# Optimization experiments

Hardware: AMD Instinct MI355X
Metric: run time of the kernel (lower is better)

The kernel has to match this reference:

```python
import jax, jax.numpy as jnp
import numpy as np

B, N, E, L, S = 8, 64, 256, 128, 2  # graphs, nodes, edges, latent dim, MPN steps


def setup_inputs() -> dict:
    key = jax.random.key(0)
    ks = jax.random.split(key, 16)

    def lin(k, fi, fo):
        return (jax.random.normal(k, (fi, fo), jnp.float32) / np.sqrt(fi).astype(np.float32))

    return {
        "x": jax.random.normal(ks[0], (B, N, L), jnp.float32),
        "edge_attr": jax.random.normal(ks[1], (B, E, L), jnp.float32),
        "u": jax.random.normal(ks[2], (B, L), jnp.float32),
        "spdist": jax.random.uniform(ks[3], (B, N, N), jnp.float32),
        "edge_index": jax.random.randint(ks[4], (B, 2, E), 0, N),
        # encoders
        "W_node_enc": lin(ks[5], 2 * L + 1, L), "b_node_enc": jnp.zeros(L, jnp.float32),
        "W_edge_enc": lin(ks[6], L, L), "b_edge_enc": jnp.zeros(L, jnp.float32),
        "W_glob_enc": lin(ks[7], L, L), "b_glob_enc": jnp.zeros(L, jnp.float32),
        # per-step edge / node update MLPs (stacked over S steps)
        "W_edge_upd": jnp.stack([lin(ks[8 + s], 4 * L, L) for s in range(S)]),
        "b_edge_upd": jnp.zeros((S, L), jnp.float32),
        "W_node_upd": jnp.stack([lin(ks[10 + s], 3 * L, L) for s in range(S)]),
        "b_node_upd": jnp.zeros((S, L), jnp.float32),
        # final edge scorer (per_dest_embedding_to_score)
        "W_score": lin(ks[12], L, 1), "b_score": jnp.zeros(1, jnp.float32),
    }


def reference(x, edge_attr, u, spdist, edge_index,
              W_node_enc, b_node_enc, W_edge_enc, b_edge_enc,
              W_glob_enc, b_glob_enc, W_edge_upd, b_edge_upd,
              W_node_upd, b_node_upd, W_score, b_score):
    act = jax.nn.leaky_relu  # torch LeakyReLU default slope 0.01
    n_steps = W_edge_upd.shape[0]

    def per_graph(xg, eg, ug, sdg, eig):
        Ng, Lg = xg.shape
        Eg = eg.shape[0]
        src, dst = eig[0], eig[1]
        # Augmented node features: graph copy d, node i -> [x_i, x_d, spdist[d, i]]
        # (matches x.repeat(N,1) / x.repeat_interleave(N,0) + chunk(N))
        x_tile = jnp.broadcast_to(xg[None, :, :], (Ng, Ng, Lg))
        x_dest = jnp.broadcast_to(xg[:, None, :], (Ng, Ng, Lg))
        xa = jnp.concatenate([x_tile, x_dest, sdg[..., None]], axis=-1)  # [Nd, N, 2L+1]
        h = act(xa @ W_node_enc + b_node_enc)                            # [Nd, N, L]
        ee = act(eg @ W_edge_enc + b_edge_enc)                           # [E, L]
        ee = jnp.broadcast_to(ee[None], (Ng, Eg, Lg))                    # [Nd, E, L]
        gg = act(ug @ W_glob_enc + b_glob_enc)                           # [L]
        for s in range(n_steps):
            gb_e = jnp.broadcast_to(gg, (Ng, Eg, Lg))
            ein = jnp.concatenate([ee, h[:, src], h[:, dst], gb_e], axis=-1)  # [Nd, E, 4L]
            ee = ee + act(ein @ W_edge_upd[s] + b_edge_upd[s])
            agg = jax.vmap(lambda ef: jax.ops.segment_sum(ef, dst, num_segments=Ng))(ee)  # [Nd, N, L]
            gb_n = jnp.broadcast_to(gg, (Ng, Ng, Lg))
            nin = jnp.concatenate([h, agg, gb_n], axis=-1)                    # [Nd, N, 3L]
            h = h + act(nin @ W_node_upd[s] + b_node_upd[s])
        scores = (ee @ W_score + b_score)[..., 0]  # [Nd, E]
        # reshape(N, -1).t().flatten() per graph -> [E * N]
        return scores.T.reshape(-1)

    out = jax.vmap(per_graph)(x, edge_attr, u, spdist, edge_index)  # [B, E*N]
    return out.reshape(-1)
```

## Files before the change

### kernel.cpp

```cpp
#include <hip/hip_runtime.h>
#include <hip/hip_bf16.h>


typedef __attribute__((ext_vector_type(8))) __bf16 bf16x8;
typedef __attribute__((ext_vector_type(4))) __bf16 bf16x4;
typedef __attribute__((ext_vector_type(4))) float  floatx4;

#define MFMA16(a, b, c) __builtin_amdgcn_mfma_f32_16x16x32_bf16((a), (b), (c), 0, 0, 0)

__device__ __forceinline__ float leaky(float x) { return x > 0.f ? x : 0.01f * x; }

#define WS_WT     0
#define WS_XAP    327680
#define WS_XDP    589824
#define WS_EE0    851968
#define WS_CE     1376256
#define WS_CN     1384448
#define WS_CSROFF 1392640
#define WS_CSREID 1394944

#define LDE 140

__global__ __launch_bounds__(256) void mpn_prep(
    const float* __restrict__ x,
    const float* __restrict__ ea,
    const float* __restrict__ u,
    const int*   __restrict__ eidx,
    const float* __restrict__ Wne,
    const float* __restrict__ bne,
    const float* __restrict__ Wee,
    const float* __restrict__ bee,
    const float* __restrict__ Wge,
    const float* __restrict__ bge,
    const float* __restrict__ Weu,
    const float* __restrict__ beu,
    const float* __restrict__ Wnu,
    const float* __restrict__ bnu,
    char* __restrict__ ws)
{
  __shared__ __align__(16) __bf16 smem[384 * LDE];

  const int b = blockIdx.x, tid = threadIdx.x;
  __bf16* wt  = (__bf16*)(ws + WS_WT);
  float*  xap = (float*)(ws + WS_XAP);
  float*  xdp = (float*)(ws + WS_XDP);
  __bf16* ee0 = (__bf16*)(ws + WS_EE0);
  float*  cev = (float*)(ws + WS_CE);
  float*  cnv = (float*)(ws + WS_CN);
  int* csroff = (int*)(ws + WS_CSROFF);
  int* csreid = (int*)(ws + WS_CSREID);

  if (b < 20) {
    const int m = b >> 1, half = b & 1;
    const int s = m / 5, t = m % 5;
    const float* src = (t < 3) ? (Weu + (size_t)(s*512 + t*128)*128)
                               : (Wnu + (size_t)(s*384 + (t-3)*128)*128);
    for (int it = 0; it < 4; ++it) {
      int p = it*256 + tid;
      int mq = half*4 + (p >> 8);
      int c  = (p >> 6) & 3;
      int l  = p & 63;
      int fr = mq*16 + (l & 15);
      int kb = c*32 + (l >> 4)*8;
      __bf16* dst = &wt[m*16384 + ((mq*4 + c)*64 + l)*8];
      #pragma unroll
      for (int j = 0; j < 8; ++j)
        dst[j] = (__bf16)src[(kb + j)*128 + fr];
    }
  } else if (b < 28) {
    const int g = b - 20;
    __shared__ float gg_sh[128];
    __shared__ int dst_sh[256];
    __shared__ int cnt_sh[64];
    __shared__ int off_sh[65];
    if (tid < 128) {
      float acc = bge[tid];
      for (int k = 0; k < 128; ++k)
        acc += u[g*128 + k] * Wge[k*128 + tid];
      gg_sh[tid] = leaky(acc);
    }
    dst_sh[tid] = eidx[g*512 + 256 + tid];
    __syncthreads();
    {
      const int s = tid >> 7, f = tid & 127;
      float ac = beu[s*128 + f];
      float an = bnu[s*128 + f];
      #pragma unroll 8
      for (int k = 0; k < 128; ++k) {
        float gk = gg_sh[k];
        ac += gk * Weu[(s*512 + 384 + k)*128 + f];
        an += gk * Wnu[(s*384 + 256 + k)*128 + f];
      }
      cev[(g*2 + s)*128 + f] = ac;
      cnv[(g*2 + s)*128 + f] = an;
    }
    if (tid < 64) {
      int c = 0;
      for (int e = 0; e < 256; ++e) c += (dst_sh[e] == tid) ? 1 : 0;
      cnt_sh[tid] = c;
    }
    __syncthreads();
    if (tid == 0) {
      int o = 0;
      for (int n = 0; n < 64; ++n) { off_sh[n] = o; o += cnt_sh[n]; }
      off_sh[64] = o;
    }
    __syncthreads();
    if (tid < 65) csroff[g*72 + tid] = off_sh[tid];
    if (tid < 64) {
      int o = off_sh[tid];
      for (int e = 0; e < 256; ++e)
        if (dst_sh[e] == tid) csreid[g*256 + (o++)] = e;
    }
  } else if (b < 36) {
    const int g = b - 28;
    __bf16* s_a = smem;
    __bf16* s_w = smem + 256*LDE;
    #pragma unroll
    for (int it = 0; it < 32; ++it) {
      int c = it*256 + tid;
      int row = c >> 5, f4 = (c & 31)*4;
      floatx4 v = *(const floatx4*)&ea[(size_t)(g*256 + row)*128 + f4];
      bf16x4 o;
      #pragma unroll
      for (int r = 0; r < 4; ++r) o[r] = (__bf16)v[r];
      *(bf16x4*)&s_a[row*LDE + f4] = o;
    }
    #pragma unroll 8
    for (int it = 0; it < 64; ++it) {
      int k = it*2 + (tid >> 7), f = tid & 127;
      s_w[f*LDE + k] = (__bf16)Wee[k*128 + f];
    }
    __syncthreads();
    const int w = tid >> 6, l = tid & 63, q = l >> 4, xn = l & 15;
    bf16x8 bea[4][4];
    #pragma unroll
    for (int t = 0; t < 4; ++t) {
      int e = w*64 + t*16 + xn;
      #pragma unroll
      for (int c = 0; c < 4; ++c)
        bea[t][c] = *(const bf16x8*)&s_a[e*LDE + c*32 + q*8];
    }
    #pragma unroll
    for (int m = 0; m < 8; ++m) {
      floatx4 acc[4];
      #pragma unroll
      for (int t = 0; t < 4; ++t) acc[t] = (floatx4)0.f;
      const int fr = m*16 + xn;
      #pragma unroll
      for (int c = 0; c < 4; ++c) {
        bf16x8 aw = *(const bf16x8*)&s_w[fr*LDE + c*32 + q*8];
        #pragma unroll
        for (int t = 0; t < 4; ++t) acc[t] = MFMA16(aw, bea[t][c], acc[t]);
      }
      const int f0 = m*16 + q*4;
      floatx4 b4 = *(const floatx4*)&bee[f0];
      #pragma unroll
      for (int t = 0; t < 4; ++t) {
        int e = w*64 + t*16 + xn;
        bf16x4 o;
        #pragma unroll
        for (int r = 0; r < 4; ++r) o[r] = (__bf16)leaky(acc[t][r] + b4[r]);
        *(bf16x4*)&ee0[(size_t)(g*256 + e)*128 + f0] = o;
      }
    }
  } else {
    const int g = b - 36;
    __bf16* s_x  = smem;
    __bf16* s_wa = smem + 64*LDE;
    __bf16* s_wb = smem + 192*LDE;
    #pragma unroll
    for (int it = 0; it < 8; ++it) {
      int c = it*256 + tid;
      int row = c >> 5, f4 = (c & 31)*4;
      floatx4 v = *(const floatx4*)&x[(size_t)(g*64 + row)*128 + f4];
      bf16x4 o;
      #pragma unroll
      for (int r = 0; r < 4; ++r) o[r] = (__bf16)v[r];
      *(bf16x4*)&s_x[row*LDE + f4] = o;
    }
    #pragma unroll 8
    for (int it = 0; it < 64; ++it) {
      int k = it*2 + (tid >> 7), f = tid & 127;
      s_wa[f*LDE + k] = (__bf16)Wne[k*128 + f];
      s_wb[f*LDE + k] = (__bf16)Wne[(128 + k)*128 + f];
    }
    __syncthreads();
    const int w = tid >> 6, l = tid & 63, q = l >> 4, xn = l & 15;
    const int i = w*16 + xn;
    bf16x8 bx[4];
    #pragma unroll
    for (int c = 0; c < 4; ++c)
      bx[c] = *(const bf16x8*)&s_x[i*LDE + c*32 + q*8];
    #pragma unroll
    for (int m = 0; m < 8; ++m) {
      floatx4 aa = (floatx4)0.f, ab = (floatx4)0.f;
      const int fr = m*16 + xn;
      #pragma unroll
      for (int c = 0; c < 4; ++c) {
        bf16x8 aw = *(const bf16x8*)&s_wa[fr*LDE + c*32 + q*8];
        aa = MFMA16(aw, bx[c], aa);
      }
      #pragma unroll
      for (int c = 0; c < 4; ++c) {
        bf16x8 aw = *(const bf16x8*)&s_wb[fr*LDE + c*32 + q*8];
        ab = MFMA16(aw, bx[c], ab);
      }
      const int f0 = m*16 + q*4;
      floatx4 bn4 = *(const floatx4*)&bne[f0];
      floatx4 oa;
      #pragma unroll
      for (int r = 0; r < 4; ++r) oa[r] = aa[r] + bn4[r];
      *(floatx4*)&xap[(size_t)(g*64 + i)*128 + f0] = oa;
      *(floatx4*)&xdp[(size_t)(g*64 + i)*128 + f0] = ab;
    }
  }
}

__global__ __launch_bounds__(512, 2) void mpn_main(
    const float* __restrict__ spdist,
    const int*   __restrict__ eidx,
    const float* __restrict__ Wne,
    const float* __restrict__ wscore,
    const float* __restrict__ bscore,
    const char* __restrict__ ws,
    float* __restrict__ out)
{
  __shared__ __align__(16) __bf16 s_ee[256*LDE];
  __shared__ __align__(16) __bf16 s_h [64*LDE];
  __shared__ __align__(16) __bf16 s_p2[64*LDE];
  __shared__ __align__(16) __bf16 s_p3[64*LDE];
  __shared__ int s_off[65];
  __shared__ int s_eid[256];
  __shared__ float s_sc[256];

  const __bf16* wt  = (const __bf16*)(ws + WS_WT);
  const float*  xap = (const float*)(ws + WS_XAP);
  const float*  xdp = (const float*)(ws + WS_XDP);
  const __bf16* ee0 = (const __bf16*)(ws + WS_EE0);
  const float*  cev = (const float*)(ws + WS_CE);
  const float*  cnv = (const float*)(ws + WS_CN);
  const int* csroff = (const int*)(ws + WS_CSROFF);
  const int* csreid = (const int*)(ws + WS_CSREID);

  const int tid = threadIdx.x;
  const int w = tid >> 6, l = tid & 63;
  const int q = l >> 4, xn = l & 15;
  const int lane8 = l*8;
  const int fme = w*16 + q*4;
  const int g = blockIdx.x >> 6, d = blockIdx.x & 63;

  if (tid < 65) s_off[tid] = csroff[g*72 + tid];
  if (tid < 256) s_eid[tid] = csreid[g*256 + tid];

  {
    const int f = tid & 127, ib = tid >> 7;
    float xdpv = xdp[(g*64 + d)*128 + f];
    float wspv = Wne[256*128 + f];
    #pragma unroll
    for (int j = 0; j < 16; ++j) {
      int i = ib + 4*j;
      float sp = spdist[(g*64 + d)*64 + i];
      float v = xap[(g*64 + i)*128 + f] + xdpv + sp*wspv;
      s_h[i*LDE + f] = (__bf16)leaky(v);
    }
  }
  #pragma unroll
  for (int it = 0; it < 8; ++it) {
    int c = it*512 + tid;
    int row = c >> 4, col = c & 15;
    *(bf16x8*)&s_ee[row*LDE + col*8] = *(const bf16x8*)&ee0[(g*256 + row)*128 + col*8];
  }

  int mySrc[16], myDst[16];
  #pragma unroll
  for (int t = 0; t < 16; ++t) {
    int e = t*16 + xn;
    mySrc[t] = eidx[g*512 + e];
    myDst[t] = eidx[g*512 + 256 + e];
  }
  __syncthreads();

  for (int s = 0; s < 2; ++s) {
    const __bf16* W1T = wt + (s*5 + 0)*16384;
    const __bf16* W2T = wt + (s*5 + 1)*16384;
    const __bf16* W3T = wt + (s*5 + 2)*16384;
    const __bf16* N1T = wt + (s*5 + 3)*16384;
    const __bf16* N2T = wt + (s*5 + 4)*16384;

    {
      bf16x8 aw2[4], aw3[4];
      #pragma unroll
      for (int c = 0; c < 4; ++c) {
        aw2[c] = *(const bf16x8*)&W2T[(w*4 + c)*512 + lane8];
        aw3[c] = *(const bf16x8*)&W3T[(w*4 + c)*512 + lane8];
      }
      floatx4 ce4 = *(const floatx4*)&cev[(g*2 + s)*128 + fme];
      #pragma unroll
      for (int t = 0; t < 4; ++t) {
        const int i = t*16 + xn;
        floatx4 a2 = (floatx4)0.f, a3 = (floatx4)0.f;
        #pragma unroll
        for (int c = 0; c < 4; ++c) {
          bf16x8 bh = *(const bf16x8*)&s_h[i*LDE + c*32 + q*8];
          a2 = MFMA16(aw2[c], bh, a2);
          a3 = MFMA16(aw3[c], bh, a3);
        }
        bf16x4 o2, o3;
        #pragma unroll
        for (int r = 0; r < 4; ++r) { o2[r] = (__bf16)a2[r]; o3[r] = (__bf16)(a3[r] + ce4[r]); }
        *(bf16x4*)&s_p2[i*LDE + fme] = o2;
        *(bf16x4*)&s_p3[i*LDE + fme] = o3;
      }
    }
    __syncthreads();

    {
      bf16x8 aw1[4];
      #pragma unroll
      for (int c = 0; c < 4; ++c)
        aw1[c] = *(const bf16x8*)&W1T[(w*4 + c)*512 + lane8];
      floatx4 acc[16];
      #pragma unroll
      for (int t = 0; t < 16; ++t) {
        const int e = t*16 + xn;
        floatx4 a = (floatx4)0.f;
        #pragma unroll
        for (int c = 0; c < 4; ++c) {
          bf16x8 be = *(const bf16x8*)&s_ee[e*LDE + c*32 + q*8];
          a = MFMA16(aw1[c], be, a);
        }
        acc[t] = a;
      }
      __syncthreads();
      #pragma unroll
      for (int t = 0; t < 16; ++t) {
        const int e = t*16 + xn;
        bf16x4 old = *(const bf16x4*)&s_ee[e*LDE + fme];
        bf16x4 v2  = *(const bf16x4*)&s_p2[mySrc[t]*LDE + fme];
        bf16x4 v3  = *(const bf16x4*)&s_p3[myDst[t]*LDE + fme];
        bf16x4 res;
        #pragma unroll
        for (int r = 0; r < 4; ++r) {
          float vv = acc[t][r] + (float)v2[r] + (float)v3[r];
          res[r] = (__bf16)((float)old[r] + leaky(vv));
        }
        *(bf16x4*)&s_ee[e*LDE + fme] = res;
      }
    }
    __syncthreads();

    if (s == 0) {
      {
        const int node = tid >> 3;
        const int fs = (tid & 7)*16;
        float av[16];
        #pragma unroll
        for (int j = 0; j < 16; ++j) av[j] = 0.f;
        const int b0 = s_off[node], b1 = s_off[node + 1];
        for (int idx = b0; idx < b1; ++idx) {
          int e = s_eid[idx];
          #pragma unroll
          for (int cc = 0; cc < 2; ++cc) {
            bf16x8 vv = *(const bf16x8*)&s_ee[e*LDE + fs + cc*8];
            #pragma unroll
            for (int j = 0; j < 8; ++j) av[cc*8 + j] += (float)vv[j];
          }
        }
        #pragma unroll
        for (int cc = 0; cc < 2; ++cc) {
          bf16x8 o;
          #pragma unroll
          for (int j = 0; j < 8; ++j) o[j] = (__bf16)av[cc*8 + j];
          *(bf16x8*)&s_p2[node*LDE + fs + cc*8] = o;
        }
      }
      __syncthreads();
      {
        bf16x8 an1[4], an2[4];
        #pragma unroll
        for (int c = 0; c < 4; ++c) {
          an1[c] = *(const bf16x8*)&N1T[(w*4 + c)*512 + lane8];
          an2[c] = *(const bf16x8*)&N2T[(w*4 + c)*512 + lane8];
        }
        floatx4 acc4[4];
        #pragma unroll
        for (int t = 0; t < 4; ++t) {
          const int i = t*16 + xn;
          floatx4 a = (floatx4)0.f;
          #pragma unroll
          for (int c = 0; c < 4; ++c) {
            bf16x8 bh = *(const bf16x8*)&s_h[i*LDE + c*32 + q*8];
            a = MFMA16(an1[c], bh, a);
          }
          #pragma unroll
          for (int c = 0; c < 4; ++c) {
            bf16x8 bg = *(const bf16x8*)&s_p2[i*LDE + c*32 + q*8];
            a = MFMA16(an2[c], bg, a);
          }
          acc4[t] = a;
        }
        __syncthreads();
        floatx4 cn4 = *(const floatx4*)&cnv[(g*2 + s)*128 + fme];
        #pragma unroll
        for (int t = 0; t < 4; ++t) {
          const int i = t*16 + xn;
          bf16x4 old = *(const bf16x4*)&s_h[i*LDE + fme];
          bf16x4 res;
          #pragma unroll
          for (int r = 0; r < 4; ++r)
            res[r] = (__bf16)((float)old[r] + leaky(acc4[t][r] + cn4[r]));
          *(bf16x4*)&s_h[i*LDE + fme] = res;
        }
      }
      __syncthreads();
    }
  }

  {
    const int e = tid & 255, hh = tid >> 8;
    float acc = 0.f;
    #pragma unroll
    for (int c = 0; c < 8; ++c) {
      bf16x8 vv = *(const bf16x8*)&s_ee[e*LDE + hh*64 + c*8];
      #pragma unroll
      for (int j = 0; j < 8; ++j) acc += (float)vv[j] * wscore[hh*64 + c*8 + j];
    }
    if (hh == 1) s_sc[e] = acc;
    __syncthreads();
    if (hh == 0) out[g*16384 + e*64 + d] = acc + s_sc[e] + bscore[0];
  }
}

extern "C" void kernel_launch(void* const* d_in, const int* in_sizes, int n_in,
                              void* d_out, int out_size, void* d_ws, size_t ws_size,
                              hipStream_t stream) {
  (void)in_sizes; (void)n_in; (void)out_size; (void)ws_size;
  const float* x   = (const float*)d_in[0];
  const float* ea  = (const float*)d_in[1];
  const float* u   = (const float*)d_in[2];
  const float* sp  = (const float*)d_in[3];
  const int*   ei  = (const int*)d_in[4];
  const float* Wne = (const float*)d_in[5];
  const float* bne = (const float*)d_in[6];
  const float* Wee = (const float*)d_in[7];
  const float* bee = (const float*)d_in[8];
  const float* Wge = (const float*)d_in[9];
  const float* bge = (const float*)d_in[10];
  const float* Weu = (const float*)d_in[11];
  const float* beu = (const float*)d_in[12];
  const float* Wnu = (const float*)d_in[13];
  const float* bnu = (const float*)d_in[14];
  const float* Wsc = (const float*)d_in[15];
  const float* bsc = (const float*)d_in[16];
  char* ws = (char*)d_ws;

  hipLaunchKernelGGL(mpn_prep, dim3(44), dim3(256), 0, stream,
                     x, ea, u, ei, Wne, bne, Wee, bee, Wge, bge, Weu, beu, Wnu, bnu, ws);
  hipLaunchKernelGGL(mpn_main, dim3(512), dim3(512), 0, stream,
                     sp, ei, Wne, Wsc, bsc, (const char*)ws, (float*)d_out);
}
```

Baseline: 158.3 us.

## Repartition edge GEMM across waves and hoist all weight fragment loads to step start

The edge-update GEMM is re-tiled so that each wave owns 64 edges and half of the 128 output features. Each wave now loads its edge tiles from shared memory once into registers and reuses them across four output-feature tiles, instead of every wave reading all 256 edge rows. All weight fragments (W1, W2, W3 and, in step 0, N1 and N2) are loaded at the start of each step so their global-memory latency overlaps earlier work. The cost is higher register pressure (w1f alone is 16 bf16x8 fragments, plus be[4][4]), which could lower occupancy or cause spills.

New measurement: 153.6 us (median of 2 runs). 3.0% less time.

```diff
diff --git a/kernel.cpp b/kernel.cpp
--- a/kernel.cpp
+++ b/kernel.cpp
@@ -246,6 +246,7 @@
   const int tid = threadIdx.x;
   const int w = tid >> 6, l = tid & 63;
   const int q = l >> 4, xn = l & 15;
+  const int wp = w >> 1, mh = w & 1;
   const int lane8 = l*8;
   const int fme = w*16 + q*4;
   const int g = blockIdx.x >> 6, d = blockIdx.x & 63;
@@ -272,10 +273,10 @@
     *(bf16x8*)&s_ee[row*LDE + col*8] = *(const bf16x8*)&ee0[(g*256 + row)*128 + col*8];
   }
 
-  int mySrc[16], myDst[16];
+  int mySrc[4], myDst[4];
   #pragma unroll
-  for (int t = 0; t < 16; ++t) {
-    int e = t*16 + xn;
+  for (int t = 0; t < 4; ++t) {
+    int e = wp*64 + t*16 + xn;
     mySrc[t] = eidx[g*512 + e];
     myDst[t] = eidx[g*512 + 256 + e];
   }
@@ -288,13 +289,26 @@
     const __bf16* N1T = wt + (s*5 + 3)*16384;
     const __bf16* N2T = wt + (s*5 + 4)*16384;
 
+    bf16x8 w2f[4], w3f[4], n1f[4], n2f[4], w1f[4][4];
+    #pragma unroll
+    for (int c = 0; c < 4; ++c) {
+      w2f[c] = *(const bf16x8*)&W2T[(w*4 + c)*512 + lane8];
+      w3f[c] = *(const bf16x8*)&W3T[(w*4 + c)*512 + lane8];
+    }
+    #pragma unroll
+    for (int mm = 0; mm < 4; ++mm)
+      #pragma unroll
+      for (int c = 0; c < 4; ++c)
+        w1f[mm][c] = *(const bf16x8*)&W1T[((mh*4 + mm)*4 + c)*512 + lane8];
+    if (s == 0) {
+      #pragma unroll
+      for (int c = 0; c < 4; ++c) {
+        n1f[c] = *(const bf16x8*)&N1T[(w*4 + c)*512 + lane8];
+        n2f[c] = *(const bf16x8*)&N2T[(w*4 + c)*512 + lane8];
+      }
+    }
+
     {
-      bf16x8 aw2[4], aw3[4];
-      #pragma unroll
-      for (int c = 0; c < 4; ++c) {
-        aw2[c] = *(const bf16x8*)&W2T[(w*4 + c)*512 + lane8];
-        aw3[c] = *(const bf16x8*)&W3T[(w*4 + c)*512 + lane8];
-      }
       floatx4 ce4 = *(const floatx4*)&cev[(g*2 + s)*128 + fme];
       #pragma unroll
       for (int t = 0; t < 4; ++t) {
@@ -303,8 +317,8 @@
         #pragma unroll
         for (int c = 0; c < 4; ++c) {
           bf16x8 bh = *(const bf16x8*)&s_h[i*LDE + c*32 + q*8];
-          a2 = MFMA16(aw2[c], bh, a2);
-          a3 = MFMA16(aw3[c], bh, a3);
+          a2 = MFMA16(w2f[c], bh, a2);
+          a3 = MFMA16(w3f[c], bh, a3);
         }
         bf16x4 o2, o3;
         #pragma unroll
@@ -316,36 +330,41 @@
     __syncthreads();
 
     {
-      bf16x8 aw1[4];
-      #pragma unroll
-      for (int c = 0; c < 4; ++c)
-        aw1[c] = *(const bf16x8*)&W1T[(w*4 + c)*512 + lane8];
-      floatx4 acc[16];
-      #pragma unroll
-      for (int t = 0; t < 16; ++t) {
-        const int e = t*16 + xn;
-        floatx4 a = (floatx4)0.f;
+      bf16x8 be[4][4];
+      #pragma unroll
+      for (int t = 0; t < 4; ++t) {
+        int e = wp*64 + t*16 + xn;
+        #pragma unroll
+        for (int c = 0; c < 4; ++c)
+          be[t][c] = *(const bf16x8*)&s_ee[e*LDE + c*32 + q*8];
+      }
+      __syncthreads();
+      #pragma unroll
+      for (int mm = 0; mm < 4; ++mm) {
+        const int m = mh*4 + mm;
+        floatx4 acc[4];
+        #pragma unroll
+        for (int t = 0; t < 4; ++t) acc[t] = (floatx4)0.f;
         #pragma unroll
         for (int c = 0; c < 4; ++c) {
-          bf16x8 be = *(const bf16x8*)&s_ee[e*LDE + c*32 + q*8];
-          a = MFMA16(aw1[c], be, a);
-        }
-        acc[t] = a;
-      }
-      __syncthreads();
-      #pragma unroll
-      for (int t = 0; t < 16; ++t) {
-        const int e = t*16 + xn;
-        bf16x4 old = *(const bf16x4*)&s_ee[e*LDE + fme];
-        bf16x4 v2  = *(const bf16x4*)&s_p2[mySrc[t]*LDE + fme];
-        bf16x4 v3  = *(const bf16x4*)&s_p3[myDst[t]*LDE + fme];
-        bf16x4 res;
-        #pragma unroll
-        for (int r = 0; r < 4; ++r) {
-          float vv = acc[t][r] + (float)v2[r] + (float)v3[r];
-          res[r] = (__bf16)((float)old[r] + leaky(vv));
-        }
-        *(bf16x4*)&s_ee[e*LDE + fme] = res;
+          #pragma unroll
+          for (int t = 0; t < 4; ++t) acc[t] = MFMA16(w1f[mm][c], be[t][c], acc[t]);
+        }
+        const int f0 = m*16 + q*4;
+        #pragma unroll
+        for (int t = 0; t < 4; ++t) {
+          int e = wp*64 + t*16 + xn;
+          bf16x4 old = *(const bf16x4*)&s_ee[e*LDE + f0];
+          bf16x4 v2  = *(const bf16x4*)&s_p2[mySrc[t]*LDE + f0];
+          bf16x4 v3  = *(const bf16x4*)&s_p3[myDst[t]*LDE + f0];
+          bf16x4 res;
+          #pragma unroll
+          for (int r = 0; r < 4; ++r) {
+            float vv = acc[t][r] + (float)v2[r] + (float)v3[r];
+            res[r] = (__bf16)((float)old[r] + leaky(vv));
+          }
+          *(bf16x4*)&s_ee[e*LDE + f0] = res;
+        }
       }
     }
     __syncthreads();
@@ -377,12 +396,6 @@
       }
       __syncthreads();
       {
-        bf16x8 an1[4], an2[4];
-        #pragma unroll
-        for (int c = 0; c < 4; ++c) {
-          an1[c] = *(const bf16x8*)&N1T[(w*4 + c)*512 + lane8];
-          an2[c] = *(const bf16x8*)&N2T[(w*4 + c)*512 + lane8];
-        }
         floatx4 acc4[4];
         #pragma unroll
         for (int t = 0; t < 4; ++t) {
@@ -391,12 +404,12 @@
           #pragma unroll
           for (int c = 0; c < 4; ++c) {
             bf16x8 bh = *(const bf16x8*)&s_h[i*LDE + c*32 + q*8];
-            a = MFMA16(an1[c], bh, a);
+            a = MFMA16(n1f[c], bh, a);
           }
           #pragma unroll
           for (int c = 0; c < 4; ++c) {
             bf16x8 bg = *(const bf16x8*)&s_p2[i*LDE + c*32 + q*8];
-            a = MFMA16(an2[c], bg, a);
+            a = MFMA16(n2f[c], bg, a);
           }
           acc4[t] = a;
         }
```
